# Kernel tuning notes

Measured on AMD Instinct MI355X. Metric: run time of the kernel, lower is better.

Reference implementation:

```python
import jax, jax.numpy as jnp
import numpy as np


def setup_inputs() -> dict:
    key = jax.random.key(0)
    ks = jax.random.split(key, 7)
    B, T, E, H = 4, 4096, 1024, 64
    return {
        "idx": jax.random.normal(ks[0], (B, T, E), dtype=jnp.float32),
        "Wq": jax.random.normal(ks[1], (E, H), dtype=jnp.float32) * (E ** -0.5),
        "bq": jax.random.normal(ks[2], (H,), dtype=jnp.float32) * 0.01,
        "Wk": jax.random.normal(ks[3], (E, H), dtype=jnp.float32) * (E ** -0.5),
        "bk": jax.random.normal(ks[4], (H,), dtype=jnp.float32) * 0.01,
        "Wv": jax.random.normal(ks[5], (E, H), dtype=jnp.float32) * (E ** -0.5),
        "bv": jax.random.normal(ks[6], (H,), dtype=jnp.float32) * 0.01,
    }


def reference(idx, Wq, bq, Wk, bk, Wv, bv):
    # idx: [B, T, E]
    d = idx.shape[-1]  # note: torch code scales by n_embd**-0.5, NOT head_size
    Q = idx @ Wq + bq  # [B, T, H]
    K = idx @ Wk + bk
    V = idx @ Wv + bv
    # scores; NOTE: original torch code calls wei.masked_fill(...) non-in-place
    # and discards the result, so no causal mask is applied. No softmax either.
    wei = jnp.einsum("bth,bsh->bts", Q, K) * (d ** -0.5)  # [B, T, T]
    out = jnp.einsum("bts,bsh->bth", wei, V)  # [B, T, H]
    return out
```

## Files before the change

### kernel.cpp

```cpp
#include <hip/hip_runtime.h>


typedef __attribute__((ext_vector_type(8))) short bf16x8;
typedef __attribute__((ext_vector_type(4))) float f32x4;

#define MFMA16(a, b, c) __builtin_amdgcn_mfma_f32_16x16x32_bf16((a), (b), (c), 0, 0, 0)

__device__ __forceinline__ unsigned short f2bf(float f) {
    unsigned int u = __float_as_uint(f);
    u += 0x7fffu + ((u >> 16) & 1u);
    return (unsigned short)(u >> 16);
}

__global__ void prep(const float* __restrict__ Wq, const float* __restrict__ Wk,
                     const float* __restrict__ Wv, unsigned short* __restrict__ WB) {
    int t = blockIdx.x * 256 + threadIdx.x;
    int kki = t / 768;
    int rem = t - kki * 768;
    int nt = rem >> 6, lane = rem & 63;
    int n = nt * 16 + (lane & 15);
    int kb = kki * 32 + ((lane >> 4) * 8);
    int mm = n >> 6, h = n & 63;
    const float* W = (mm == 0) ? Wq : (mm == 1) ? Wk : Wv;
    float sc = (mm == 1) ? 0.03125f : 1.0f;
    bf16x8 v;
    #pragma unroll
    for (int j = 0; j < 8; j++) v[j] = (short)f2bf(W[(size_t)(kb + j) * 64 + h] * sc);
    *(bf16x8*)(WB + (size_t)t * 8) = v;
}

__global__ __launch_bounds__(256, 2) void qkv(
    const float* __restrict__ idx, const unsigned short* __restrict__ WB,
    const float* __restrict__ bq, const float* __restrict__ bk, const float* __restrict__ bv,
    unsigned short* __restrict__ Q, unsigned short* __restrict__ Kt,
    unsigned short* __restrict__ Vt) {
    __shared__ unsigned short As[32 * 1032];
    const int lane = threadIdx.x & 63, w = threadIdx.x >> 6;
    const int r0 = blockIdx.x * 32;

    const float* src = idx + (size_t)(r0 + w * 8) * 1024;
    #pragma unroll
    for (int batch = 0; batch < 4; batch++) {
        float4 v[8];
        #pragma unroll
        for (int j = 0; j < 8; j++)
            v[j] = *(const float4*)(src + (size_t)(batch * 8 + j) * 256 + lane * 4);
        #pragma unroll
        for (int j = 0; j < 8; j++) {
            int i   = batch * 8 + j;
            int row = w * 8 + (i >> 2);
            int k   = (i & 3) * 256 + lane * 4;
            unsigned int lo = ((unsigned int)f2bf(v[j].y) << 16) | f2bf(v[j].x);
            unsigned int hi = ((unsigned int)f2bf(v[j].w) << 16) | f2bf(v[j].z);
            uint2 p; p.x = lo; p.y = hi;
            *(uint2*)(As + (size_t)row * 1032 + k) = p;
        }
    }
    __syncthreads();

    const f32x4 z4 = {0.f, 0.f, 0.f, 0.f};
    f32x4 acc[2][3];
    #pragma unroll
    for (int mt = 0; mt < 2; mt++)
        #pragma unroll
        for (int j = 0; j < 3; j++) acc[mt][j] = z4;

    const int al = lane & 15;
    const int kq = (lane >> 4) * 8;
    #pragma unroll 4
    for (int kk = 0; kk < 32; kk++) {
        bf16x8 a0 = *(const bf16x8*)(As + (size_t)al * 1032 + kk * 32 + kq);
        bf16x8 a1 = *(const bf16x8*)(As + (size_t)(16 + al) * 1032 + kk * 32 + kq);
        const unsigned short* Bp = WB + (size_t)((kk * 12) * 64 + lane) * 8;
        #pragma unroll
        for (int j = 0; j < 3; j++) {
            int nt = w + j * 4;
            bf16x8 bb = *(const bf16x8*)(Bp + nt * 512);
            acc[0][j] = MFMA16(a0, bb, acc[0][j]);
            acc[1][j] = MFMA16(a1, bb, acc[1][j]);
        }
    }

    const int h = w * 16 + (lane & 15);
    #pragma unroll
    for (int j = 0; j < 3; j++) {
        float bias = (j == 0) ? bq[h] : (j == 1) ? bk[h] * 0.03125f : bv[h];
        #pragma unroll
        for (int mt = 0; mt < 2; mt++) {
            int rbase = r0 + mt * 16 + (lane >> 4) * 4;
            #pragma unroll
            for (int reg = 0; reg < 4; reg++) {
                int r = rbase + reg;
                unsigned short v = f2bf(acc[mt][j][reg] + bias);
                if (j == 0) {
                    Q[(size_t)r * 64 + h] = v;
                } else {
                    int b = r >> 12, t = r & 4095;
                    unsigned short* dst = (j == 1) ? Kt : Vt;
                    dst[(size_t)b * 262144 + h * 4096 + t] = v;
                }
            }
        }
    }
}

__global__ __launch_bounds__(256) void ktv_partial(
    const unsigned short* __restrict__ Kt, const unsigned short* __restrict__ Vt,
    float* __restrict__ part) {
    const int lane = threadIdx.x & 63, wave = threadIdx.x >> 6;
    const int c = blockIdx.x, b = blockIdx.y;
    const unsigned short* Kb = Kt + (size_t)b * 262144;
    const unsigned short* Vb = Vt + (size_t)b * 262144;
    const f32x4 z4 = {0.f, 0.f, 0.f, 0.f};
    f32x4 acc[4] = {z4, z4, z4, z4};
    const int m  = 16 * wave + (lane & 15);
    const int tq = (lane >> 4) * 8;
    #pragma unroll
    for (int it = 0; it < 4; it++) {
        int t0 = c * 128 + it * 32 + tq;
        bf16x8 a = *(const bf16x8*)&Kb[(size_t)m * 4096 + t0];
        #pragma unroll
        for (int nt = 0; nt < 4; nt++) {
            bf16x8 bb = *(const bf16x8*)&Vb[(size_t)(nt * 16 + (lane & 15)) * 4096 + t0];
            acc[nt] = MFMA16(a, bb, acc[nt]);
        }
    }
    float* P = part + (size_t)(b * 32 + c) * 4096;
    const int rowb = 16 * wave + (lane >> 4) * 4;
    #pragma unroll
    for (int nt = 0; nt < 4; nt++)
        #pragma unroll
        for (int reg = 0; reg < 4; reg++)
            P[(rowb + reg) * 64 + nt * 16 + (lane & 15)] = acc[nt][reg];
}

__global__ void reduce_m(const float* __restrict__ part,
                         unsigned short* __restrict__ Mt) {
    int i = blockIdx.x * 256 + threadIdx.x;
    int b = i >> 12, h1 = (i >> 6) & 63, h2 = i & 63;
    float s = 0.f;
    #pragma unroll
    for (int cc = 0; cc < 32; cc++)
        s += part[(size_t)(b * 32 + cc) * 4096 + h1 * 64 + h2];
    Mt[(size_t)b * 4096 + h2 * 64 + h1] = f2bf(s);
}

__global__ __launch_bounds__(256) void qm(
    const unsigned short* __restrict__ Q, const unsigned short* __restrict__ Mt,
    float* __restrict__ out) {
    const int lane = threadIdx.x & 63, wave = threadIdx.x >> 6;
    const int r0 = blockIdx.x * 64;
    const int b  = r0 >> 12;
    const f32x4 z4 = {0.f, 0.f, 0.f, 0.f};
    f32x4 acc[4] = {z4, z4, z4, z4};
    const int rr = r0 + 16 * wave + (lane & 15);
    const int kq = (lane >> 4) * 8;
    #pragma unroll
    for (int ks = 0; ks < 2; ks++) {
        int k0 = ks * 32;
        bf16x8 a = *(const bf16x8*)&Q[(size_t)rr * 64 + k0 + kq];
        #pragma unroll
        for (int nt = 0; nt < 4; nt++) {
            bf16x8 bb = *(const bf16x8*)&Mt[(size_t)b * 4096 + (nt * 16 + (lane & 15)) * 64 + k0 + kq];
            acc[nt] = MFMA16(a, bb, acc[nt]);
        }
    }
    const int rowb = r0 + 16 * wave + (lane >> 4) * 4;
    #pragma unroll
    for (int nt = 0; nt < 4; nt++)
        #pragma unroll
        for (int reg = 0; reg < 4; reg++)
            out[(size_t)(rowb + reg) * 64 + nt * 16 + (lane & 15)] = acc[nt][reg];
}

extern "C" void kernel_launch(void* const* d_in, const int* in_sizes, int n_in,
                              void* d_out, int out_size, void* d_ws, size_t ws_size,
                              hipStream_t stream) {
    const float* idx = (const float*)d_in[0];
    const float* Wq  = (const float*)d_in[1];
    const float* bq  = (const float*)d_in[2];
    const float* Wk  = (const float*)d_in[3];
    const float* bk  = (const float*)d_in[4];
    const float* Wv  = (const float*)d_in[5];
    const float* bv  = (const float*)d_in[6];
    float* out = (float*)d_out;

    char* ws = (char*)d_ws;
    unsigned short* WB = (unsigned short*)(ws);
    float*          Pp = (float*)(ws);
    unsigned short* Q  = (unsigned short*)(ws + (2048u << 10));
    unsigned short* Kt = (unsigned short*)(ws + (4096u << 10));
    unsigned short* Vt = (unsigned short*)(ws + (6144u << 10));
    unsigned short* Mt = (unsigned short*)(ws + (8192u << 10));

    hipLaunchKernelGGL(prep,        dim3(96),     dim3(256), 0, stream, Wq, Wk, Wv, WB);
    hipLaunchKernelGGL(qkv,         dim3(512),    dim3(256), 0, stream,
                       idx, WB, bq, bk, bv, Q, Kt, Vt);
    hipLaunchKernelGGL(ktv_partial, dim3(32, 4),  dim3(256), 0, stream, Kt, Vt, Pp);
    hipLaunchKernelGGL(reduce_m,    dim3(64),     dim3(256), 0, stream, Pp, Mt);
    hipLaunchKernelGGL(qm,          dim3(256),    dim3(256), 0, stream, Q, Mt, out);
}
```

Before: 128.2 us.

## Halve QKV row tile, prefetch operands, stage outputs through LDS for coalesced stores

The QKV projection kernel now handles 16 rows per block instead of 32, doubling the grid and halving LDS use so that more blocks can be resident (launch bounds raised to 4). The inner K loop register double-buffers the next A and B fragments ahead of the MFMAs. Outputs are staged in shared memory so the transposed K and V writes become coalesced vector stores instead of scattered 2-byte stores. The cost is that each weight fragment is now reused across only one MFMA row tile, so weight reads from cache double.

New measurement: 125.7 us (median of 2 runs). -2.0%, faster.

```diff
diff --git a/kernel.cpp b/kernel.cpp
--- a/kernel.cpp
+++ b/kernel.cpp
@@ -29,18 +29,18 @@
     *(bf16x8*)(WB + (size_t)t * 8) = v;
 }
 
-__global__ __launch_bounds__(256, 2) void qkv(
+__global__ __launch_bounds__(256, 4) void qkv(
     const float* __restrict__ idx, const unsigned short* __restrict__ WB,
     const float* __restrict__ bq, const float* __restrict__ bk, const float* __restrict__ bv,
     unsigned short* __restrict__ Q, unsigned short* __restrict__ Kt,
     unsigned short* __restrict__ Vt) {
-    __shared__ unsigned short As[32 * 1032];
+    __shared__ unsigned short As[16 * 1032];
     const int lane = threadIdx.x & 63, w = threadIdx.x >> 6;
-    const int r0 = blockIdx.x * 32;
-
-    const float* src = idx + (size_t)(r0 + w * 8) * 1024;
-    #pragma unroll
-    for (int batch = 0; batch < 4; batch++) {
+    const int r0 = blockIdx.x * 16;
+
+    const float* src = idx + (size_t)(r0 + w * 4) * 1024;
+    #pragma unroll
+    for (int batch = 0; batch < 2; batch++) {
         float4 v[8];
         #pragma unroll
         for (int j = 0; j < 8; j++)
@@ -48,7 +48,7 @@
         #pragma unroll
         for (int j = 0; j < 8; j++) {
             int i   = batch * 8 + j;
-            int row = w * 8 + (i >> 2);
+            int row = w * 4 + (i >> 2);
             int k   = (i & 3) * 256 + lane * 4;
             unsigned int lo = ((unsigned int)f2bf(v[j].y) << 16) | f2bf(v[j].x);
             unsigned int hi = ((unsigned int)f2bf(v[j].w) << 16) | f2bf(v[j].z);
@@ -59,48 +59,58 @@
     __syncthreads();
 
     const f32x4 z4 = {0.f, 0.f, 0.f, 0.f};
-    f32x4 acc[2][3];
-    #pragma unroll
-    for (int mt = 0; mt < 2; mt++)
-        #pragma unroll
-        for (int j = 0; j < 3; j++) acc[mt][j] = z4;
-
-    const int al = lane & 15;
-    const int kq = (lane >> 4) * 8;
-    #pragma unroll 4
+    f32x4 acc[3] = {z4, z4, z4};
+
+    const unsigned short* a_base = As + (size_t)(lane & 15) * 1032 + ((lane >> 4) * 8);
+    bf16x8 a_c = *(const bf16x8*)(a_base);
+    bf16x8 bc[3], bn[3];
+    {
+        const unsigned short* Bp = WB + (size_t)(lane * 8);
+        #pragma unroll
+        for (int j = 0; j < 3; j++) bc[j] = *(const bf16x8*)(Bp + (w + j * 4) * 512);
+    }
     for (int kk = 0; kk < 32; kk++) {
-        bf16x8 a0 = *(const bf16x8*)(As + (size_t)al * 1032 + kk * 32 + kq);
-        bf16x8 a1 = *(const bf16x8*)(As + (size_t)(16 + al) * 1032 + kk * 32 + kq);
-        const unsigned short* Bp = WB + (size_t)((kk * 12) * 64 + lane) * 8;
-        #pragma unroll
-        for (int j = 0; j < 3; j++) {
-            int nt = w + j * 4;
-            bf16x8 bb = *(const bf16x8*)(Bp + nt * 512);
-            acc[0][j] = MFMA16(a0, bb, acc[0][j]);
-            acc[1][j] = MFMA16(a1, bb, acc[1][j]);
-        }
-    }
-
-    const int h = w * 16 + (lane & 15);
-    #pragma unroll
-    for (int j = 0; j < 3; j++) {
-        float bias = (j == 0) ? bq[h] : (j == 1) ? bk[h] * 0.03125f : bv[h];
-        #pragma unroll
-        for (int mt = 0; mt < 2; mt++) {
-            int rbase = r0 + mt * 16 + (lane >> 4) * 4;
+        bf16x8 a_n = a_c;
+        if (kk < 31) {
+            const unsigned short* Bp = WB + (size_t)(((kk + 1) * 12) * 64 + lane) * 8;
             #pragma unroll
-            for (int reg = 0; reg < 4; reg++) {
-                int r = rbase + reg;
-                unsigned short v = f2bf(acc[mt][j][reg] + bias);
-                if (j == 0) {
-                    Q[(size_t)r * 64 + h] = v;
-                } else {
-                    int b = r >> 12, t = r & 4095;
-                    unsigned short* dst = (j == 1) ? Kt : Vt;
-                    dst[(size_t)b * 262144 + h * 4096 + t] = v;
-                }
-            }
-        }
+            for (int j = 0; j < 3; j++) bn[j] = *(const bf16x8*)(Bp + (w + j * 4) * 512);
+            a_n = *(const bf16x8*)(a_base + (kk + 1) * 32);
+        }
+        #pragma unroll
+        for (int j = 0; j < 3; j++) acc[j] = MFMA16(a_c, bc[j], acc[j]);
+        #pragma unroll
+        for (int j = 0; j < 3; j++) bc[j] = bn[j];
+        a_c = a_n;
+    }
+
+    __syncthreads();
+    unsigned short* Lq = As;
+    unsigned short* Lk = As + 1024;
+    unsigned short* Lv = As + 2048;
+    const int h   = w * 16 + (lane & 15);
+    const int row = (lane >> 4) * 4;
+    {
+        float bias0 = bq[h], bias1 = bk[h] * 0.03125f, bias2 = bv[h];
+        #pragma unroll
+        for (int reg = 0; reg < 4; reg++) {
+            int r = row + reg;
+            Lq[r * 64 + h] = f2bf(acc[0][reg] + bias0);
+            Lk[h * 16 + r] = f2bf(acc[1][reg] + bias1);
+            Lv[h * 16 + r] = f2bf(acc[2][reg] + bias2);
+        }
+    }
+    __syncthreads();
+    {
+        const int tt = threadIdx.x;
+        int qr = tt >> 4, qh = (tt & 15) * 4;
+        *(uint2*)(Q + (size_t)(r0 + qr) * 64 + qh) = *(const uint2*)(Lq + qr * 64 + qh);
+        int b = r0 >> 12, t0 = r0 & 4095;
+        int hh = tt >> 2, tc = (tt & 3) * 4;
+        *(uint2*)(Kt + (size_t)b * 262144 + hh * 4096 + t0 + tc) =
+            *(const uint2*)(Lk + hh * 16 + tc);
+        *(uint2*)(Vt + (size_t)b * 262144 + hh * 4096 + t0 + tc) =
+            *(const uint2*)(Lv + hh * 16 + tc);
     }
 }
 
@@ -194,7 +204,7 @@
     unsigned short* Mt = (unsigned short*)(ws + (8192u << 10));
 
     hipLaunchKernelGGL(prep,        dim3(96),     dim3(256), 0, stream, Wq, Wk, Wv, WB);
-    hipLaunchKernelGGL(qkv,         dim3(512),    dim3(256), 0, stream,
+    hipLaunchKernelGGL(qkv,         dim3(1024),   dim3(256), 0, stream,
                        idx, WB, bq, bk, bv, Q, Kt, Vt);
     hipLaunchKernelGGL(ktv_partial, dim3(32, 4),  dim3(256), 0, stream, Kt, Vt, Pp);
     hipLaunchKernelGGL(reduce_m,    dim3(64),     dim3(256), 0, stream, Pp, Mt);
```
